# Optimization experiments

Hardware: AMD Instinct MI355X
Metric: run time of the kernel (lower is better)

The kernel has to match this reference:

```python
import jax, jax.numpy as jnp
import numpy as np
from jax.scipy.special import logsumexp

NUM_CLASSES = 200
NUM_PROTOTYPES = 10
EMBED_DIM = 512
QUEUE_SIZE = 8192
MOMENTUM = 0.02
ITERATIONS = 5
EPSILON = 0.01
EPS_LOG = 1e-8


def _l2norm(x):
    return x / jnp.linalg.norm(x, axis=-1, keepdims=True)


def setup_inputs() -> dict:
    key = jax.random.key(0)
    k1, k2, k3 = jax.random.split(key, 3)
    tokens = jax.random.normal(k1, (QUEUE_SIZE, EMBED_DIM), dtype=jnp.float32)
    labels = jax.random.randint(k2, (QUEUE_SIZE,), 0, NUM_CLASSES, dtype=jnp.int64)
    # prototypes buffer is xavier-init then L2-normalized in __init__
    protos = jax.random.normal(k3, (NUM_CLASSES * NUM_PROTOTYPES, EMBED_DIM), dtype=jnp.float32)
    prototypes = _l2norm(protos)
    return {"tokens": tokens, "labels": labels, "prototypes": prototypes}


def mask_sinkhorn(C, mask, row_group_size, col_group_size, iterations, epsilon):
    # C: [P, N] cost, mask: [P, N] bool; log-domain masked Sinkhorn
    log_a = jnp.log(1.0 / row_group_size + EPS_LOG)  # [P]
    log_b = jnp.log(1.0 / col_group_size + EPS_LOG)  # [N]
    neg_inf = jnp.float32(-jnp.inf)

    def kernel(u, v):
        # (-C + u_i + v_j)/eps on mask, -inf off mask
        return jnp.where(mask, (-C + u[:, None] + v[None, :]) / epsilon, neg_inf)

    u = jnp.zeros(C.shape[0], dtype=C.dtype)
    v = jnp.zeros(C.shape[1], dtype=C.dtype)
    for _ in range(iterations):
        u_ = log_a - logsumexp(kernel(u, v), axis=1)
        u = epsilon * jnp.nan_to_num(u_, posinf=0.0) + u
        v_ = log_b - logsumexp(kernel(u, v), axis=0)
        v = epsilon * jnp.nan_to_num(v_, posinf=0.0) + v
    return jnp.exp(kernel(u, v))  # transport plan pi [P, N]


def reference(tokens, labels, prototypes):
    tok = _l2norm(tokens)  # normalize=True
    P = NUM_CLASSES * NUM_PROTOTYPES
    proto_class_id = jnp.repeat(jnp.arange(NUM_CLASSES), NUM_PROTOTYPES)  # [P]
    # group sizes (counts of same class among prototypes / among labels)
    row_group_size = jnp.full((P,), float(NUM_PROTOTYPES), dtype=jnp.float32)
    counts = jnp.bincount(labels, length=NUM_CLASSES)
    col_group_size = counts[labels].astype(jnp.float32)  # [N]
    mask = proto_class_id[:, None] == labels[None, :]  # [P, N]
    C = -(prototypes @ tok.T)  # [P, N]
    pi = mask_sinkhorn(C, mask, row_group_size, col_group_size, ITERATIONS, EPSILON)
    pi_ = pi / pi.sum(0, keepdims=True)
    new_prototypes = pi_ @ tok  # [P, D]
    out = (1.0 - MOMENTUM) * prototypes + MOMENTUM * new_prototypes
    return _l2norm(out)
```

## Files before the change

kernel.cpp:

```cpp
#include <hip/hip_runtime.h>
#include <math.h>

#define NUM_CLASSES 200
#define NUM_PROTO   10
#define EMBED_D     512
#define NTOK        8192
#define INV_EPS     100.0f
#define EPSF        0.01f
#define MOM         0.02f
#define ITERS       5
#define CAPJ        256

__device__ __forceinline__ float wave_sum(float v) {
#pragma unroll
    for (int o = 32; o; o >>= 1) v += __shfl_xor(v, o);
    return v;
}
__device__ __forceinline__ float wave_max(float v) {
#pragma unroll
    for (int o = 32; o; o >>= 1) v = fmaxf(v, __shfl_xor(v, o));
    return v;
}

__global__ __launch_bounds__(1024) void k_all(
        const float* __restrict__ tokens,
        const int*   __restrict__ labels,
        const float* __restrict__ protos,
        float*       __restrict__ out) {
    __shared__ float S_sh[NUM_PROTO][CAPJ];
    __shared__ float red[16][NUM_PROTO][128];
    __shared__ float o_sh[NUM_PROTO][EMBED_D];
    __shared__ float v_sh[CAPJ];
    __shared__ float inv_l[CAPJ];
    __shared__ float u_sh[NUM_PROTO];
    __shared__ int   idx_l[CAPJ];
    __shared__ int   weq[16];

    const int c    = blockIdx.x;
    const int tid  = threadIdx.x;
    const int lane = tid & 63;
    const int wave = tid >> 6;

    int4 la = *(const int4*)(labels + tid * 8);
    int4 lb = *(const int4*)(labels + tid * 8 + 4);
    int l[8] = {la.x, la.y, la.z, la.w, lb.x, lb.y, lb.z, lb.w};
    int meq = 0;
#pragma unroll
    for (int i = 0; i < 8; ++i) meq += (l[i] == c);
    int incl = meq;
#pragma unroll
    for (int o = 1; o < 64; o <<= 1) { int t = __shfl_up(incl, o); if (lane >= o) incl += t; }
    if (lane == 63) weq[wave] = incl;
    if (tid < CAPJ) v_sh[tid] = 0.0f;
    __syncthreads();
    int cnt = 0, wbase = 0;
#pragma unroll
    for (int w = 0; w < 16; ++w) { int q = weq[w]; cnt += q; if (w < wave) wbase += q; }
    if (cnt > CAPJ) cnt = CAPJ;
    int pos = wbase + incl - meq;
#pragma unroll
    for (int i = 0; i < 8; ++i)
        if (l[i] == c && pos < CAPJ) { idx_l[pos] = tid * 8 + i; ++pos; }
    __syncthreads();

    {
        const int wp = wave >> 1, ph = wave & 1;
        float preg[5][8];
        const float* pb = protos + (size_t)(c * NUM_PROTO + ph * 5) * EMBED_D + lane * 8;
#pragma unroll
        for (int p = 0; p < 5; ++p) {
            float4 x = *(const float4*)(pb + p * EMBED_D);
            float4 y = *(const float4*)(pb + p * EMBED_D + 4);
            preg[p][0]=x.x; preg[p][1]=x.y; preg[p][2]=x.z; preg[p][3]=x.w;
            preg[p][4]=y.x; preg[p][5]=y.y; preg[p][6]=y.z; preg[p][7]=y.w;
        }
        for (int j = wp; j < cnt; j += 8) {
            int n = idx_l[j];
            const float* tr = tokens + (size_t)n * EMBED_D + lane * 8;
            float4 ta = *(const float4*)tr;
            float4 tb = *(const float4*)(tr + 4);
            float ssq = ta.x*ta.x + ta.y*ta.y + ta.z*ta.z + ta.w*ta.w
                      + tb.x*tb.x + tb.y*tb.y + tb.z*tb.z + tb.w*tb.w;
            ssq = wave_sum(ssq);
            float inv = 1.0f / sqrtf(ssq);
            if (ph == 0 && lane == 0) inv_l[j] = inv;
#pragma unroll
            for (int p = 0; p < 5; ++p) {
                float d = preg[p][0]*ta.x + preg[p][1]*ta.y + preg[p][2]*ta.z + preg[p][3]*ta.w
                        + preg[p][4]*tb.x + preg[p][5]*tb.y + preg[p][6]*tb.z + preg[p][7]*tb.w;
                d = wave_sum(d);
                if (lane == 0) S_sh[ph * 5 + p][j] = d * inv;
            }
        }
    }
    __syncthreads();

    const float log_a = -2.3025850f;
    const float log_b = __logf(1.0f / (float)(cnt > 0 ? cnt : 1) + 1e-8f);
    for (int it = 0; it < ITERS; ++it) {
        if (wave < NUM_PROTO) {
            int j1 = lane + 64, j2 = lane + 128, j3 = lane + 192;
            float x0 = (lane < cnt) ? (S_sh[wave][lane] + v_sh[lane]) * INV_EPS : -1e30f;
            float x1 = (j1  < cnt) ? (S_sh[wave][j1]  + v_sh[j1])  * INV_EPS : -1e30f;
            float x2 = (j2  < cnt) ? (S_sh[wave][j2]  + v_sh[j2])  * INV_EPS : -1e30f;
            float x3 = (j3  < cnt) ? (S_sh[wave][j3]  + v_sh[j3])  * INV_EPS : -1e30f;
            float M  = wave_max(fmaxf(fmaxf(x0, x1), fmaxf(x2, x3)));
            float sm = wave_sum(__expf(x0 - M) + __expf(x1 - M)
                              + __expf(x2 - M) + __expf(x3 - M));
            if (lane == 0) u_sh[wave] = EPSF * (log_a - (M + __logf(sm)));
        }
        __syncthreads();
        if (tid < cnt) {
            float x[NUM_PROTO], m = -1e30f;
#pragma unroll
            for (int p = 0; p < NUM_PROTO; ++p) {
                x[p] = (S_sh[p][tid] + u_sh[p]) * INV_EPS;
                m = fmaxf(m, x[p]);
            }
            float sm = 0.0f;
#pragma unroll
            for (int p = 0; p < NUM_PROTO; ++p) sm += __expf(x[p] - m);
            v_sh[tid] = EPSF * (log_b - (m + __logf(sm)));
        }
        __syncthreads();
    }
    if (tid < cnt) {
        float vj = v_sh[tid];
        float e[NUM_PROTO], cs = 0.0f;
#pragma unroll
        for (int p = 0; p < NUM_PROTO; ++p) {
            e[p] = __expf((S_sh[p][tid] + u_sh[p] + vj) * INV_EPS);
            cs += e[p];
        }
        float sc = inv_l[tid] / cs;
#pragma unroll
        for (int p = 0; p < NUM_PROTO; ++p) S_sh[p][tid] = e[p] * sc;
    }
    __syncthreads();

    const int g  = wave >> 2, js = wave & 3;
    const int d0 = g * 128 + lane * 2;
    float acc[NUM_PROTO][2];
#pragma unroll
    for (int p = 0; p < NUM_PROTO; ++p) { acc[p][0] = 0.0f; acc[p][1] = 0.0f; }
    for (int j = js; j < cnt; j += 4) {
        int n = idx_l[j];
        float2 t = *(const float2*)(tokens + (size_t)n * EMBED_D + d0);
#pragma unroll
        for (int p = 0; p < NUM_PROTO; ++p) {
            float w = S_sh[p][j];
            acc[p][0] += w * t.x;
            acc[p][1] += w * t.y;
        }
    }
#pragma unroll
    for (int p = 0; p < NUM_PROTO; ++p)
        *(float2*)&red[wave][p][lane * 2] = make_float2(acc[p][0], acc[p][1]);
    __syncthreads();

    for (int e4 = tid; e4 < NUM_PROTO * EMBED_D; e4 += 1024) {
        int p  = e4 >> 9;
        int d  = e4 & 511;
        int gg = d >> 7;
        int dd = d & 127;
        float s = red[gg * 4 + 0][p][dd] + red[gg * 4 + 1][p][dd]
                + red[gg * 4 + 2][p][dd] + red[gg * 4 + 3][p][dd];
        int row = c * NUM_PROTO + p;
        o_sh[p][d] = (1.0f - MOM) * protos[(size_t)row * EMBED_D + d] + MOM * s;
    }
    __syncthreads();

    if (wave < NUM_PROTO) {
        const float* orow = &o_sh[wave][0];
        float4 a = *(const float4*)(orow + lane * 8);
        float4 b = *(const float4*)(orow + lane * 8 + 4);
        float ss = a.x*a.x + a.y*a.y + a.z*a.z + a.w*a.w
                 + b.x*b.x + b.y*b.y + b.z*b.z + b.w*b.w;
        ss = wave_sum(ss);
        float inv = 1.0f / sqrtf(ss);
        int row = c * NUM_PROTO + wave;
        float* od = out + (size_t)row * EMBED_D + lane * 8;
        float4 w0 = make_float4(a.x*inv, a.y*inv, a.z*inv, a.w*inv);
        float4 w1 = make_float4(b.x*inv, b.y*inv, b.z*inv, b.w*inv);
        *(float4*)od       = w0;
        *(float4*)(od + 4) = w1;
    }
}

extern "C" void kernel_launch(void* const* d_in, const int* in_sizes, int n_in,
                              void* d_out, int out_size, void* d_ws, size_t ws_size,
                              hipStream_t stream) {
    const float* tokens = (const float*)d_in[0];
    const int*   labels = (const int*)d_in[1];
    const float* protos = (const float*)d_in[2];
    float* out = (float*)d_out;
    (void)d_ws; (void)ws_size; (void)in_sizes; (void)n_in; (void)out_size;

    k_all<<<NUM_CLASSES, 1024, 0, stream>>>(tokens, labels, protos, out);
}
```

Measured before the change: 34.36 us.

## Shrink per-class token cap, prefetch token rows, fold last Sinkhorn v-step

New measurement: 33.93 us. About the same (-1.3%).

```diff
diff --git a/kernel.cpp b/kernel.cpp
--- a/kernel.cpp
+++ b/kernel.cpp
@@ -9,7 +9,7 @@
 #define EPSF        0.01f
 #define MOM         0.02f
 #define ITERS       5
-#define CAPJ        256
+#define CAPJ        128
 
 __device__ __forceinline__ float wave_sum(float v) {
 #pragma unroll
@@ -74,11 +74,21 @@
             preg[p][0]=x.x; preg[p][1]=x.y; preg[p][2]=x.z; preg[p][3]=x.w;
             preg[p][4]=y.x; preg[p][5]=y.y; preg[p][6]=y.z; preg[p][7]=y.w;
         }
-        for (int j = wp; j < cnt; j += 8) {
-            int n = idx_l[j];
-            const float* tr = tokens + (size_t)n * EMBED_D + lane * 8;
-            float4 ta = *(const float4*)tr;
-            float4 tb = *(const float4*)(tr + 4);
+        int j = wp;
+        float4 ta, tb;
+        if (j < cnt) {
+            const float* tr = tokens + (size_t)idx_l[j] * EMBED_D + lane * 8;
+            ta = *(const float4*)tr;
+            tb = *(const float4*)(tr + 4);
+        }
+        while (j < cnt) {
+            int j2 = j + 8;
+            float4 na, nb;
+            if (j2 < cnt) {
+                const float* tr = tokens + (size_t)idx_l[j2] * EMBED_D + lane * 8;
+                na = *(const float4*)tr;
+                nb = *(const float4*)(tr + 4);
+            }
             float ssq = ta.x*ta.x + ta.y*ta.y + ta.z*ta.z + ta.w*ta.w
                       + tb.x*tb.x + tb.y*tb.y + tb.z*tb.z + tb.w*tb.w;
             ssq = wave_sum(ssq);
@@ -91,6 +101,7 @@
                 d = wave_sum(d);
                 if (lane == 0) S_sh[ph * 5 + p][j] = d * inv;
             }
+            ta = na; tb = nb; j = j2;
         }
     }
     __syncthreads();
@@ -99,39 +110,40 @@
     const float log_b = __logf(1.0f / (float)(cnt > 0 ? cnt : 1) + 1e-8f);
     for (int it = 0; it < ITERS; ++it) {
         if (wave < NUM_PROTO) {
-            int j1 = lane + 64, j2 = lane + 128, j3 = lane + 192;
+            int j1 = lane + 64;
             float x0 = (lane < cnt) ? (S_sh[wave][lane] + v_sh[lane]) * INV_EPS : -1e30f;
             float x1 = (j1  < cnt) ? (S_sh[wave][j1]  + v_sh[j1])  * INV_EPS : -1e30f;
-            float x2 = (j2  < cnt) ? (S_sh[wave][j2]  + v_sh[j2])  * INV_EPS : -1e30f;
-            float x3 = (j3  < cnt) ? (S_sh[wave][j3]  + v_sh[j3])  * INV_EPS : -1e30f;
-            float M  = wave_max(fmaxf(fmaxf(x0, x1), fmaxf(x2, x3)));
-            float sm = wave_sum(__expf(x0 - M) + __expf(x1 - M)
-                              + __expf(x2 - M) + __expf(x3 - M));
+            float M  = wave_max(fmaxf(x0, x1));
+            float sm = wave_sum(__expf(x0 - M) + __expf(x1 - M));
             if (lane == 0) u_sh[wave] = EPSF * (log_a - (M + __logf(sm)));
         }
         __syncthreads();
-        if (tid < cnt) {
-            float x[NUM_PROTO], m = -1e30f;
-#pragma unroll
-            for (int p = 0; p < NUM_PROTO; ++p) {
-                x[p] = (S_sh[p][tid] + u_sh[p]) * INV_EPS;
-                m = fmaxf(m, x[p]);
+        if (it < ITERS - 1) {
+            if (tid < cnt) {
+                float x[NUM_PROTO], m = -1e30f;
+#pragma unroll
+                for (int p = 0; p < NUM_PROTO; ++p) {
+                    x[p] = (S_sh[p][tid] + u_sh[p]) * INV_EPS;
+                    m = fmaxf(m, x[p]);
+                }
+                float sm = 0.0f;
+#pragma unroll
+                for (int p = 0; p < NUM_PROTO; ++p) sm += __expf(x[p] - m);
+                v_sh[tid] = EPSF * (log_b - (m + __logf(sm)));
             }
-            float sm = 0.0f;
-#pragma unroll
-            for (int p = 0; p < NUM_PROTO; ++p) sm += __expf(x[p] - m);
-            v_sh[tid] = EPSF * (log_b - (m + __logf(sm)));
-        }
-        __syncthreads();
+            __syncthreads();
+        }
     }
     if (tid < cnt) {
-        float vj = v_sh[tid];
+        float x[NUM_PROTO], m = -1e30f;
+#pragma unroll
+        for (int p = 0; p < NUM_PROTO; ++p) {
+            x[p] = (S_sh[p][tid] + u_sh[p]) * INV_EPS;
+            m = fmaxf(m, x[p]);
+        }
         float e[NUM_PROTO], cs = 0.0f;
 #pragma unroll
-        for (int p = 0; p < NUM_PROTO; ++p) {
-            e[p] = __expf((S_sh[p][tid] + u_sh[p] + vj) * INV_EPS);
-            cs += e[p];
-        }
+        for (int p = 0; p < NUM_PROTO; ++p) { e[p] = __expf(x[p] - m); cs += e[p]; }
         float sc = inv_l[tid] / cs;
 #pragma unroll
         for (int p = 0; p < NUM_PROTO; ++p) S_sh[p][tid] = e[p] * sc;
```
